# Performance work log

Measured on AMD Instinct MI355X. Metric: run time of the kernel, lower is better.

The kernel has to match this reference:

```python
import jax, jax.numpy as jnp
import numpy as np

N = 800          # atoms
F = 128          # n_filters / embedding dim
G = 50           # n_gaussians
L_INT = 3        # n_interactions
CUTOFF = 5.0     # Angstrom
BOX_NM = 2.3     # box edge in nm (positions are in nm, scaled *10 inside)
LOG2 = 0.6931471805599453


def ssp(x):
    # shifted softplus used throughout schnetpack
    return jax.nn.softplus(x) - LOG2


def setup_inputs() -> dict:
    key = jax.random.key(0)
    ks = jax.random.split(key, 20)
    s = 0.05
    inp = {
        "positions": jax.random.uniform(ks[0], (N, 3), jnp.float32) * BOX_NM,
        "boxvectors": (BOX_NM * jnp.eye(3)).astype(jnp.float32),
        "atomic_numbers": jax.random.randint(ks[1], (N,), 1, 10),
        "embedding": jax.random.normal(ks[2], (100, F), jnp.float32) * s,
        # filter-generating network (per interaction, stacked on leading dim)
        "Wf1": jax.random.normal(ks[3], (L_INT, G, F), jnp.float32) * s,
        "bf1": jnp.zeros((L_INT, F), jnp.float32),
        "Wf2": jax.random.normal(ks[4], (L_INT, F, F), jnp.float32) * s,
        "bf2": jnp.zeros((L_INT, F), jnp.float32),
        # cfconv in2f (no bias) and post-aggregation dense layers
        "Win": jax.random.normal(ks[5], (L_INT, F, F), jnp.float32) * s,
        "W2": jax.random.normal(ks[6], (L_INT, F, F), jnp.float32) * s,
        "b2": jnp.zeros((L_INT, F), jnp.float32),
        "W3": jax.random.normal(ks[7], (L_INT, F, F), jnp.float32) * s,
        "b3": jnp.zeros((L_INT, F), jnp.float32),
        # Atomwise output head (F -> F//2 -> 1)
        "Wo1": jax.random.normal(ks[8], (F, F // 2), jnp.float32) * s,
        "bo1": jnp.zeros((F // 2,), jnp.float32),
        "Wo2": jax.random.normal(ks[9], (F // 2, 1), jnp.float32) * s,
        "bo2": jnp.zeros((1,), jnp.float32),
    }
    return inp


def reference(positions, boxvectors, atomic_numbers, embedding,
              Wf1, bf1, Wf2, bf2, Win, W2, b2, W3, b3,
              Wo1, bo1, Wo2, bo2):
    # nm -> Angstrom, as in the original forward
    pos = positions * 10.0
    cell = boxvectors * 10.0

    # PBC pairwise displacements via minimum image (box > 2*cutoff, so exact
    # equivalent of the shift-based neighbor list within the cutoff)
    d = pos[:, None, :] - pos[None, :, :]                  # [N,N,3]
    inv_cell = jnp.linalg.inv(cell)
    frac = d @ inv_cell
    frac = frac - jnp.round(frac)
    d = frac @ cell

    eye = jnp.eye(pos.shape[0], dtype=bool)
    r2 = jnp.sum(d * d, axis=-1)
    r = jnp.sqrt(jnp.where(eye, 1.0, r2))                  # safe sqrt on diag
    nbr_mask = (r < CUTOFF) & (~eye)                       # neighbor_mask
    fmask = nbr_mask.astype(pos.dtype)

    # gaussian RBF expansion on [0, cutoff]
    centers = jnp.linspace(0.0, CUTOFF, G, dtype=pos.dtype)
    width = centers[1] - centers[0]
    gamma = 0.5 / (width * width)
    g = jnp.exp(-gamma * (r[..., None] - centers) ** 2) * fmask[..., None]  # [N,N,G]

    # SchNet interactions
    x = embedding[atomic_numbers]                           # [N,F]
    for l in range(L_INT):
        # continuous filters W_ij from distances
        Wij = ssp(jnp.einsum('ijg,gf->ijf', g, Wf1[l]) + bf1[l])
        Wij = (jnp.einsum('ijf,fk->ijk', Wij, Wf2[l]) + bf2[l]) * fmask[..., None]
        xf = x @ Win[l]                                     # in2f
        m = jnp.einsum('ijf,jf->if', Wij, xf)               # gather-weight-scatter
        v = ssp(m @ W2[l] + b2[l]) @ W3[l] + b3[l]
        x = x + v                                           # residual update

    # Atomwise energy head, sum-pooled to total potential
    e_atom = ssp(x @ Wo1 + bo1) @ Wo2 + bo2                 # [N,1]
    return jnp.sum(e_atom)
```

## Files before the change

kernel.cpp:

```cpp
#include <hip/hip_runtime.h>

#define SN_NA    800
#define SN_F     128
#define SN_G     50
#define SN_MAXP  16384
#define SN_MAXN  128
#define SN_CUT2  25.0f

typedef __attribute__((ext_vector_type(4))) float f32x4;
typedef __attribute__((ext_vector_type(8))) short short8;

#define OB_BF1 0
#define OB_BF2 384
#define OB_B2  768
#define OB_B3  1152
#define OB_BO1 1536
#define OB_WO2 1600
#define OB_BO2 1664
#define NB_TOT 1665

#define OT_WF1T 0
#define OT_WF2T 24576
#define OT_W2T  73728
#define OT_W3T  122880
#define OT_WINT 172032
#define OT_WO1T 221184
#define NT_TOT  229376

#define WO_PCNT  0
#define WO_DONE  32
#define WO_NCLO  64
#define WO_NCUP  3264
#define WO_NBRP  6464
#define WO_NBRO  416064
#define WO_PAIRR 825664
#define WO_WB    891200
#define WO_WTT   897872
#define WO_WPH   1356624
#define WO_X     13939536
#define WO_XF    14349136
#define WO_XF2   14758736
#define WO_EPART 15168336
#define SN_WSNEED (WO_EPART + 256)

__device__ __forceinline__ float ldr(const void* p, int idx, int bf) {
    if (bf) {
        unsigned int x = ((unsigned int)(((const unsigned short*)p)[idx])) << 16;
        float f; __builtin_memcpy(&f, &x, 4); return f;
    }
    return ((const float*)p)[idx];
}
__device__ __forceinline__ int bfflag(const void* box) {
    float b0 = ((const float*)box)[0];
    return !(b0 > 1e-3f && b0 < 1e3f);
}
__device__ __forceinline__ float bf2f(unsigned short u) {
    unsigned int x = ((unsigned int)u) << 16;
    float f; __builtin_memcpy(&f, &x, 4); return f;
}
__device__ __forceinline__ unsigned short f2bf(float v) {
    unsigned int b; __builtin_memcpy(&b, &v, 4);
    return (unsigned short)((b + 0x7FFFu + ((b >> 16) & 1u)) >> 16);
}
__device__ __forceinline__ float sspf(float v) {
    float sp = fmaxf(v, 0.0f) + log1pf(__expf(-fabsf(v)));
    return sp - 0.69314718055994530942f;
}

__global__ void k_prep(const void* pos, const void* box,
                       const void* bf1w, const void* bf2w, const void* b2m, const void* b3m,
                       const void* bo1w, const void* wo2w, const void* bo2w,
                       const void* wf1, const void* wf2, const void* w2m, const void* w3m,
                       const void* winm, const void* wo1,
                       float* wb, unsigned short* wtT,
                       int* pcnt, int* ncup, int* nclo,
                       int* nbrp, int* nbro, float* pairr) {
    __shared__ int   lj[64];
    __shared__ float lr[64];
    __shared__ int   lsh[2];
    int bf = bfflag(box);
    int bid = blockIdx.x, tid = threadIdx.x;

    if (bid < 7) {
        int t = bid * 256 + tid;
        if (t < NB_TOT) {
            const int   sz[7] = {384,384,384,384,64,64,1};
            const void* ps[7] = {bf1w,bf2w,b2m,b3m,bo1w,wo2w,bo2w};
            int rem = t, s = 0;
#pragma unroll
            for (int q = 0; q < 7; q++) { if (rem >= sz[q]) { rem -= sz[q]; s = q+1; } else break; }
            wb[t] = ldr(ps[s], rem, bf);
        }
        return;
    }
    if (bid < 903) {
        int t = (bid - 7) * 256 + tid;
        if (t < NT_TOT) {
            float v;
            if (t < OT_WF2T) {
                int lay = t / 8192, rem = t - lay*8192, col = rem >> 6, k = rem & 63;
                v = (k < SN_G) ? ldr(wf1, lay*(SN_G*SN_F) + k*SN_F + col, bf) : 0.0f;
            } else if (t < OT_W2T) {
                int i2 = t - OT_WF2T; int lay = i2 >> 14, rem = i2 & 16383, col = rem >> 7, k = rem & 127;
                v = ldr(wf2, lay*16384 + k*128 + col, bf);
            } else if (t < OT_W3T) {
                int i2 = t - OT_W2T;  int lay = i2 >> 14, rem = i2 & 16383, col = rem >> 7, k = rem & 127;
                v = ldr(w2m, lay*16384 + k*128 + col, bf);
            } else if (t < OT_WINT) {
                int i2 = t - OT_W3T;  int lay = i2 >> 14, rem = i2 & 16383, col = rem >> 7, k = rem & 127;
                v = ldr(w3m, lay*16384 + k*128 + col, bf);
            } else if (t < OT_WO1T) {
                int i2 = t - OT_WINT; int lay = i2 >> 14, rem = i2 & 16383, col = rem >> 7, k = rem & 127;
                v = ldr(winm, lay*16384 + k*128 + col, bf);
            } else {
                int i2 = t - OT_WO1T; int col = i2 >> 7, k = i2 & 127;
                v = ldr(wo1, k*64 + col, bf);
            }
            wtT[t] = f2bf(v);
        }
        return;
    }

    int i = bid - 903;
    if (tid == 0) lsh[0] = 0;
    float c00 = ldr(box,0,bf)*10.f, c01 = ldr(box,1,bf)*10.f, c02 = ldr(box,2,bf)*10.f;
    float c10 = ldr(box,3,bf)*10.f, c11 = ldr(box,4,bf)*10.f, c12 = ldr(box,5,bf)*10.f;
    float c20 = ldr(box,6,bf)*10.f, c21 = ldr(box,7,bf)*10.f, c22 = ldr(box,8,bf)*10.f;
    float det = c00*(c11*c22 - c12*c21) - c01*(c10*c22 - c12*c20) + c02*(c10*c21 - c11*c20);
    float id  = 1.0f / det;
    float i00 = (c11*c22 - c12*c21)*id, i01 = (c02*c21 - c01*c22)*id, i02 = (c01*c12 - c02*c11)*id;
    float i10 = (c12*c20 - c10*c22)*id, i11 = (c00*c22 - c02*c20)*id, i12 = (c02*c10 - c00*c12)*id;
    float i20 = (c10*c21 - c11*c20)*id, i21 = (c01*c20 - c00*c21)*id, i22 = (c00*c11 - c01*c10)*id;
    float xi = ldr(pos, i*3+0, bf)*10.f;
    float yi = ldr(pos, i*3+1, bf)*10.f;
    float zi = ldr(pos, i*3+2, bf)*10.f;
    __syncthreads();

    for (int j = i + 1 + tid; j < SN_NA; j += 256) {
        float dx = xi - ldr(pos, j*3+0, bf)*10.f;
        float dy = yi - ldr(pos, j*3+1, bf)*10.f;
        float dz = zi - ldr(pos, j*3+2, bf)*10.f;
        float fx = dx*i00 + dy*i10 + dz*i20;
        float fy = dx*i01 + dy*i11 + dz*i21;
        float fz = dx*i02 + dy*i12 + dz*i22;
        fx -= rintf(fx); fy -= rintf(fy); fz -= rintf(fz);
        float ax = fx*c00 + fy*c10 + fz*c20;
        float ay = fx*c01 + fy*c11 + fz*c21;
        float az = fx*c02 + fy*c12 + fz*c22;
        float r2 = ax*ax + ay*ay + az*az;
        if (r2 < SN_CUT2) {
            int k = atomicAdd(&lsh[0], 1);
            if (k < 64) { lj[k] = j; lr[k] = sqrtf(r2); }
        }
    }
    __syncthreads();

    int cnt = lsh[0]; if (cnt > 64) cnt = 64;
    if (tid == 0) lsh[1] = atomicAdd(pcnt, cnt);
    __syncthreads();
    int base = lsh[1];
    int avail = SN_MAXP - base; if (avail < 0) avail = 0;
    int stored = cnt < avail ? cnt : avail;
    if (tid == 0) ncup[i] = stored;

    if (tid < stored) {
        int p = base + tid;
        int j = lj[tid];
        pairr[p] = lr[tid];
        nbrp[i*SN_MAXN + tid] = p;
        nbro[i*SN_MAXN + tid] = j;
        int kj = atomicAdd(&nclo[j], 1);
        if (kj < 64) {
            nbrp[j*SN_MAXN + 64 + kj] = p;
            nbro[j*SN_MAXN + 64 + kj] = i;
        }
    }
}

__global__ void k_initfilter(const int* zn, const void* emb, const void* box,
                             const float* pairr, const int* pcnt,
                             const float* wb, const unsigned short* wtT,
                             float* x, float* xf, unsigned short* wph) {
    __shared__ unsigned short es[16][136];
    __shared__ unsigned short gls[16][72];
    __shared__ unsigned short hls[16][136];
    int tid  = threadIdx.x;
    int lane = tid & 63;
    int wave = tid >> 6;
    int rowA = lane & 15;
    int kgrp = lane >> 4;

    if (blockIdx.x < 50) {
        int bf = bfflag(box);
        int a0 = blockIdx.x * 16;
        int a = tid >> 4, f0 = (tid & 15) * 8;
        int atom = a0 + a;
        int z = zn[atom];
        float v[8];
#pragma unroll
        for (int q = 0; q < 8; q++) v[q] = ldr(emb, z*SN_F + f0 + q, bf);
        *(float4*)&x[atom*SN_F + f0]     = make_float4(v[0],v[1],v[2],v[3]);
        *(float4*)&x[atom*SN_F + f0 + 4] = make_float4(v[4],v[5],v[6],v[7]);
#pragma unroll
        for (int q = 0; q < 8; q++) es[a][f0+q] = f2bf(v[q]);
        __syncthreads();

        int c0 = wave * 32;
        f32x4 acc0 = {0.f,0.f,0.f,0.f}, acc1 = {0.f,0.f,0.f,0.f};
        const unsigned short* wn = wtT + OT_WINT;
#pragma unroll
        for (int ks = 0; ks < 4; ks++) {
            short8 a8 = *(const short8*)&es[rowA][ks*32 + kgrp*8];
            short8 w0 = *(const short8*)(wn + (c0 + rowA)*128      + ks*32 + kgrp*8);
            short8 w1 = *(const short8*)(wn + (c0 + 16 + rowA)*128 + ks*32 + kgrp*8);
            acc0 = __builtin_amdgcn_mfma_f32_16x16x32_bf16(a8, w0, acc0, 0, 0, 0);
            acc1 = __builtin_amdgcn_mfma_f32_16x16x32_bf16(a8, w1, acc1, 0, 0, 0);
        }
#pragma unroll
        for (int r = 0; r < 4; r++) {
            int row = kgrp*4 + r;
            xf[(a0 + row)*SN_F + c0 + rowA]      = acc0[r];
            xf[(a0 + row)*SN_F + c0 + 16 + rowA] = acc1[r];
        }
        return;
    }

    int fb  = blockIdx.x - 50;
    int lay = fb >> 10;
    int p0  = (fb & 1023) * 16;
    int cnt = *pcnt; if (cnt > SN_MAXP) cnt = SN_MAXP;
    if (p0 >= cnt) return;
    int c0 = wave * 32;

    {
        int pr = tid >> 4, k0 = (tid & 15) * 4;
        int p = p0 + pr;
        float r = (p < cnt) ? pairr[p] : -1.0f;
        const float width = 5.0f/49.0f, gamma = 0.5f/(width*width);
        unsigned short gv[4];
#pragma unroll
        for (int q = 0; q < 4; q++) {
            int k = k0 + q;
            float g = 0.f;
            if (k < SN_G && r >= 0.f) { float d = r - width*(float)k; g = __expf(-gamma*d*d); }
            gv[q] = f2bf(g);
        }
        *(unsigned long long*)&gls[pr][k0] = *(unsigned long long*)gv;
    }
    __syncthreads();

    f32x4 acc0 = {0.f,0.f,0.f,0.f}, acc1 = {0.f,0.f,0.f,0.f};
    const unsigned short* b1 = wtT + OT_WF1T + lay*8192;
#pragma unroll
    for (int ks = 0; ks < 2; ks++) {
        short8 a8 = *(const short8*)&gls[rowA][ks*32 + kgrp*8];
        short8 w0 = *(const short8*)(b1 + (c0 + rowA)*64      + ks*32 + kgrp*8);
        short8 w1 = *(const short8*)(b1 + (c0 + 16 + rowA)*64 + ks*32 + kgrp*8);
        acc0 = __builtin_amdgcn_mfma_f32_16x16x32_bf16(a8, w0, acc0, 0, 0, 0);
        acc1 = __builtin_amdgcn_mfma_f32_16x16x32_bf16(a8, w1, acc1, 0, 0, 0);
    }
    {
        float b1c0 = wb[OB_BF1 + lay*SN_F + c0 + rowA];
        float b1c1 = wb[OB_BF1 + lay*SN_F + c0 + 16 + rowA];
#pragma unroll
        for (int r = 0; r < 4; r++) {
            int row = kgrp*4 + r;
            hls[row][c0 + rowA]      = f2bf(sspf(acc0[r] + b1c0));
            hls[row][c0 + 16 + rowA] = f2bf(sspf(acc1[r] + b1c1));
        }
    }
    __syncthreads();

    f32x4 d0 = {0.f,0.f,0.f,0.f}, d1 = {0.f,0.f,0.f,0.f};
    const unsigned short* b2w = wtT + OT_WF2T + lay*16384;
#pragma unroll
    for (int ks = 0; ks < 4; ks++) {
        short8 a8 = *(const short8*)&hls[rowA][ks*32 + kgrp*8];
        short8 w0 = *(const short8*)(b2w + (c0 + rowA)*128      + ks*32 + kgrp*8);
        short8 w1 = *(const short8*)(b2w + (c0 + 16 + rowA)*128 + ks*32 + kgrp*8);
        d0 = __builtin_amdgcn_mfma_f32_16x16x32_bf16(a8, w0, d0, 0, 0, 0);
        d1 = __builtin_amdgcn_mfma_f32_16x16x32_bf16(a8, w1, d1, 0, 0, 0);
    }
    {
        unsigned short* wout = wph + lay*(SN_MAXP*SN_F);
        float b2c0 = wb[OB_BF2 + lay*SN_F + c0 + rowA];
        float b2c1 = wb[OB_BF2 + lay*SN_F + c0 + 16 + rowA];
#pragma unroll
        for (int r = 0; r < 4; r++) {
            int p = p0 + kgrp*4 + r;
            wout[p*SN_F + c0 + rowA]      = f2bf(d0[r] + b2c0);
            wout[p*SN_F + c0 + 16 + rowA] = f2bf(d1[r] + b2c1);
        }
    }
}

__global__ void k_layerM(const int* ncup, const int* nclo,
                         const int* nbrp, const int* nbro,
                         const unsigned short* wph, const float* xf_in, float* x,
                         const float* wb, const unsigned short* wtT,
                         int lay, int layNext, float* xf_out,
                         float* epart, int* done, const void* box, void* out) {
    __shared__ int   spA[16][128], sjA[16][128];
    __shared__ unsigned short ms[16][136], ts[16][136], xs[16][136];
    __shared__ float red[512];
    __shared__ int   lastf;
    int tid = threadIdx.x;
    int a0 = blockIdx.x * 16;
    int a = tid >> 5, l32 = tid & 31;
    int atom = a0 + a;
    int up = ncup[atom]; if (up > 64) up = 64;
    int lo = nclo[atom]; if (lo > 64) lo = 64;
    int cn = up + lo;
    for (int k = l32; k < up; k += 32) {
        spA[a][k] = nbrp[atom*SN_MAXN + k];
        sjA[a][k] = nbro[atom*SN_MAXN + k];
    }
    for (int k = l32; k < lo; k += 32) {
        spA[a][up + k] = nbrp[atom*SN_MAXN + 64 + k];
        sjA[a][up + k] = nbro[atom*SN_MAXN + 64 + k];
    }
    __syncthreads();

    {
        int f0 = l32 * 4;
        float acc[4] = {0.f,0.f,0.f,0.f};
        const unsigned short* wpb = wph + lay*(SN_MAXP*SN_F);
        int k = 0;
        for (; k + 2 <= cn; k += 2) {
            int p0 = spA[a][k],   j0 = sjA[a][k];
            int p1 = spA[a][k+1], j1 = sjA[a][k+1];
            ushort4 w0 = *(const ushort4*)(wpb + p0*SN_F + f0);
            ushort4 w1 = *(const ushort4*)(wpb + p1*SN_F + f0);
            float4  xa = *(const float4*)(xf_in + j0*SN_F + f0);
            float4  xb = *(const float4*)(xf_in + j1*SN_F + f0);
            acc[0] = fmaf(bf2f(w0.x), xa.x, fmaf(bf2f(w1.x), xb.x, acc[0]));
            acc[1] = fmaf(bf2f(w0.y), xa.y, fmaf(bf2f(w1.y), xb.y, acc[1]));
            acc[2] = fmaf(bf2f(w0.z), xa.z, fmaf(bf2f(w1.z), xb.z, acc[2]));
            acc[3] = fmaf(bf2f(w0.w), xa.w, fmaf(bf2f(w1.w), xb.w, acc[3]));
        }
        if (k < cn) {
            int p0 = spA[a][k], j0 = sjA[a][k];
            ushort4 w0 = *(const ushort4*)(wpb + p0*SN_F + f0);
            float4  xa = *(const float4*)(xf_in + j0*SN_F + f0);
            acc[0] = fmaf(bf2f(w0.x), xa.x, acc[0]);
            acc[1] = fmaf(bf2f(w0.y), xa.y, acc[1]);
            acc[2] = fmaf(bf2f(w0.z), xa.z, acc[2]);
            acc[3] = fmaf(bf2f(w0.w), xa.w, acc[3]);
        }
#pragma unroll
        for (int q = 0; q < 4; q++) ms[a][f0+q] = f2bf(acc[q]);
    }
    __syncthreads();

    int lane = tid & 63;
    int wave = tid >> 6;
    int c0   = wave * 16;
    int rowA = lane & 15;
    int kgrp = lane >> 4;
    int col  = c0 + rowA;

    {
        f32x4 acc = {0.f,0.f,0.f,0.f};
        const unsigned short* w = wtT + OT_W2T + lay*16384;
#pragma unroll
        for (int ks = 0; ks < 4; ks++) {
            short8 a8 = *(const short8*)&ms[rowA][ks*32 + kgrp*8];
            short8 w8 = *(const short8*)(w + col*128 + ks*32 + kgrp*8);
            acc = __builtin_amdgcn_mfma_f32_16x16x32_bf16(a8, w8, acc, 0, 0, 0);
        }
        float bc = wb[OB_B2 + lay*SN_F + col];
#pragma unroll
        for (int r = 0; r < 4; r++) ts[kgrp*4 + r][col] = f2bf(sspf(acc[r] + bc));
    }
    __syncthreads();

    {
        f32x4 acc = {0.f,0.f,0.f,0.f};
        const unsigned short* w = wtT + OT_W3T + lay*16384;
#pragma unroll
        for (int ks = 0; ks < 4; ks++) {
            short8 a8 = *(const short8*)&ts[rowA][ks*32 + kgrp*8];
            short8 w8 = *(const short8*)(w + col*128 + ks*32 + kgrp*8);
            acc = __builtin_amdgcn_mfma_f32_16x16x32_bf16(a8, w8, acc, 0, 0, 0);
        }
        float bc = wb[OB_B3 + lay*SN_F + col];
#pragma unroll
        for (int r = 0; r < 4; r++) {
            int row = kgrp*4 + r;
            float xnew = x[(a0 + row)*SN_F + col] + acc[r] + bc;
            x[(a0 + row)*SN_F + col] = xnew;
            xs[row][col] = f2bf(xnew);
        }
    }
    __syncthreads();

    if (layNext >= 0) {
        f32x4 acc = {0.f,0.f,0.f,0.f};
        const unsigned short* w = wtT + OT_WINT + layNext*16384;
#pragma unroll
        for (int ks = 0; ks < 4; ks++) {
            short8 a8 = *(const short8*)&xs[rowA][ks*32 + kgrp*8];
            short8 w8 = *(const short8*)(w + col*128 + ks*32 + kgrp*8);
            acc = __builtin_amdgcn_mfma_f32_16x16x32_bf16(a8, w8, acc, 0, 0, 0);
        }
#pragma unroll
        for (int r = 0; r < 4; r++)
            xf_out[(a0 + kgrp*4 + r)*SN_F + col] = acc[r];
        return;
    }

    float e = 0.f;
    if (wave < 4) {
        f32x4 H = {0.f,0.f,0.f,0.f};
        const unsigned short* w = wtT + OT_WO1T;
#pragma unroll
        for (int ks = 0; ks < 4; ks++) {
            short8 a8 = *(const short8*)&xs[rowA][ks*32 + kgrp*8];
            short8 w8 = *(const short8*)(w + col*128 + ks*32 + kgrp*8);
            H = __builtin_amdgcn_mfma_f32_16x16x32_bf16(a8, w8, H, 0, 0, 0);
        }
        float bo = wb[OB_BO1 + col];
        float wo = wb[OB_WO2 + col];
#pragma unroll
        for (int r = 0; r < 4; r++) e += sspf(H[r] + bo) * wo;
    }
    red[tid] = e;
    __syncthreads();
    for (int wd = 256; wd > 0; wd >>= 1) {
        if (tid < wd) red[tid] += red[tid + wd];
        __syncthreads();
    }
    if (tid == 0) {
        epart[blockIdx.x] = red[0];
        __threadfence();
        int old = atomicAdd(done, 1);
        lastf = (old == 49);
    }
    __syncthreads();
    if (lastf) {
        __threadfence();
        if (tid < 64) {
            float s = (tid < 50) ? epart[tid] : 0.f;
#pragma unroll
            for (int off = 32; off > 0; off >>= 1) s += __shfl_down(s, off, 64);
            if (tid == 0) {
                float v = s + (float)SN_NA * wb[OB_BO2];
                if (bfflag(box)) ((unsigned short*)out)[0] = f2bf(v);
                else             ((float*)out)[0] = v;
            }
        }
    }
}

__global__ void k_fail(void* out) {
    ((unsigned short*)out)[0] = 0x449A;
}

extern "C" void kernel_launch(void* const* d_in, const int* in_sizes, int n_in,
                              void* d_out, int out_size, void* d_ws, size_t ws_size,
                              hipStream_t stream)
{
    const void* pos = d_in[0];
    const void* box = d_in[1];
    const int*  zn  = (const int*)d_in[2];
    const void* emb = d_in[3];

    if (ws_size < (size_t)SN_WSNEED) {
        k_fail<<<1, 1, 0, stream>>>(d_out);
        return;
    }

    char* ws = (char*)d_ws;
    int*            pcnt  = (int*)           (ws + WO_PCNT);
    int*            done  = (int*)           (ws + WO_DONE);
    int*            nclo  = (int*)           (ws + WO_NCLO);
    int*            ncup  = (int*)           (ws + WO_NCUP);
    int*            nbrp  = (int*)           (ws + WO_NBRP);
    int*            nbro  = (int*)           (ws + WO_NBRO);
    float*          pairr = (float*)         (ws + WO_PAIRR);
    float*          wb    = (float*)         (ws + WO_WB);
    unsigned short* wtT   = (unsigned short*)(ws + WO_WTT);
    unsigned short* wph   = (unsigned short*)(ws + WO_WPH);
    float*          x     = (float*)         (ws + WO_X);
    float*          xfA   = (float*)         (ws + WO_XF);
    float*          xfB   = (float*)         (ws + WO_XF2);
    float*          epart = (float*)         (ws + WO_EPART);

    hipMemsetAsync(ws, 0, 3264, stream);

    k_prep<<<1703, 256, 0, stream>>>(pos, box,
        d_in[5], d_in[7], d_in[10], d_in[12], d_in[14], d_in[15], d_in[16],
        d_in[4], d_in[6], d_in[9], d_in[11], d_in[8], d_in[13],
        wb, wtT, pcnt, ncup, nclo, nbrp, nbro, pairr);

    k_initfilter<<<50 + 3*1024, 256, 0, stream>>>(zn, emb, box, pairr, pcnt,
                                                  wb, wtT, x, xfA, wph);

    float* xf_in = xfA;
    float* xf_out = xfB;
    for (int l = 0; l < 3; l++) {
        int layNext = (l < 2) ? (l + 1) : -1;
        k_layerM<<<50, 512, 0, stream>>>(ncup, nclo, nbrp, nbro, wph, xf_in, x,
                                         wb, wtT, l, layNext, xf_out,
                                         epart, done, box, d_out);
        float* t = xf_in; xf_in = xf_out; xf_out = t;
    }
}
```

Baseline: 95.79 us.

## Pack neighbor lists and split layer kernel into 100 blocks of 8 atoms

The pair index and neighbor atom index are packed into a single 32-bit word, which halves neighbor-list storage and the loads needed to fill it. The per-layer kernel now runs 100 blocks of 256 threads, each covering 8 atoms instead of 16, so twice as many CUs take part in the memory-bound gather phase. The MFMA stages now compute 32 columns per wave and zero-pad the unused 8 rows of the 16-row tile, which wastes half the matrix work. The final energy reduction is adapted to 100 partial sums.

```diff
diff --git a/kernel.cpp b/kernel.cpp
--- a/kernel.cpp
+++ b/kernel.cpp
@@ -31,8 +31,7 @@
 #define WO_DONE  32
 #define WO_NCLO  64
 #define WO_NCUP  3264
-#define WO_NBRP  6464
-#define WO_NBRO  416064
+#define WO_NBR   6464
 #define WO_PAIRR 825664
 #define WO_WB    891200
 #define WO_WTT   897872
@@ -41,7 +40,7 @@
 #define WO_XF    14349136
 #define WO_XF2   14758736
 #define WO_EPART 15168336
-#define SN_WSNEED (WO_EPART + 256)
+#define SN_WSNEED (WO_EPART + 512)
 
 __device__ __forceinline__ float ldr(const void* p, int idx, int bf) {
     if (bf) {
@@ -74,7 +73,7 @@
                        const void* winm, const void* wo1,
                        float* wb, unsigned short* wtT,
                        int* pcnt, int* ncup, int* nclo,
-                       int* nbrp, int* nbro, float* pairr) {
+                       unsigned int* nbr, float* pairr) {
     __shared__ int   lj[64];
     __shared__ float lr[64];
     __shared__ int   lsh[2];
@@ -167,13 +166,9 @@
         int p = base + tid;
         int j = lj[tid];
         pairr[p] = lr[tid];
-        nbrp[i*SN_MAXN + tid] = p;
-        nbro[i*SN_MAXN + tid] = j;
+        nbr[i*SN_MAXN + tid] = ((unsigned int)p << 10) | (unsigned int)j;
         int kj = atomicAdd(&nclo[j], 1);
-        if (kj < 64) {
-            nbrp[j*SN_MAXN + 64 + kj] = p;
-            nbro[j*SN_MAXN + 64 + kj] = i;
-        }
+        if (kj < 64) nbr[j*SN_MAXN + 64 + kj] = ((unsigned int)p << 10) | (unsigned int)i;
     }
 }
 
@@ -295,30 +290,28 @@
 }
 
 __global__ void k_layerM(const int* ncup, const int* nclo,
-                         const int* nbrp, const int* nbro,
+                         const unsigned int* nbr,
                          const unsigned short* wph, const float* xf_in, float* x,
                          const float* wb, const unsigned short* wtT,
                          int lay, int layNext, float* xf_out,
                          float* epart, int* done, const void* box, void* out) {
-    __shared__ int   spA[16][128], sjA[16][128];
+    __shared__ unsigned int nl[8][128];
     __shared__ unsigned short ms[16][136], ts[16][136], xs[16][136];
-    __shared__ float red[512];
+    __shared__ float red[256];
     __shared__ int   lastf;
     int tid = threadIdx.x;
-    int a0 = blockIdx.x * 16;
+    int a0 = blockIdx.x * 8;
     int a = tid >> 5, l32 = tid & 31;
     int atom = a0 + a;
     int up = ncup[atom]; if (up > 64) up = 64;
     int lo = nclo[atom]; if (lo > 64) lo = 64;
     int cn = up + lo;
-    for (int k = l32; k < up; k += 32) {
-        spA[a][k] = nbrp[atom*SN_MAXN + k];
-        sjA[a][k] = nbro[atom*SN_MAXN + k];
-    }
-    for (int k = l32; k < lo; k += 32) {
-        spA[a][up + k] = nbrp[atom*SN_MAXN + 64 + k];
-        sjA[a][up + k] = nbro[atom*SN_MAXN + 64 + k];
-    }
+    for (int k = l32; k < up; k += 32) nl[a][k]      = nbr[atom*SN_MAXN + k];
+    for (int k = l32; k < lo; k += 32) nl[a][up + k] = nbr[atom*SN_MAXN + 64 + k];
+    ms[8 + (tid >> 5)][(tid & 31)*4 + 0] = 0;
+    ms[8 + (tid >> 5)][(tid & 31)*4 + 1] = 0;
+    ms[8 + (tid >> 5)][(tid & 31)*4 + 2] = 0;
+    ms[8 + (tid >> 5)][(tid & 31)*4 + 3] = 0;
     __syncthreads();
 
     {
@@ -327,21 +320,20 @@
         const unsigned short* wpb = wph + lay*(SN_MAXP*SN_F);
         int k = 0;
         for (; k + 2 <= cn; k += 2) {
-            int p0 = spA[a][k],   j0 = sjA[a][k];
-            int p1 = spA[a][k+1], j1 = sjA[a][k+1];
-            ushort4 w0 = *(const ushort4*)(wpb + p0*SN_F + f0);
-            ushort4 w1 = *(const ushort4*)(wpb + p1*SN_F + f0);
-            float4  xa = *(const float4*)(xf_in + j0*SN_F + f0);
-            float4  xb = *(const float4*)(xf_in + j1*SN_F + f0);
+            unsigned int v0 = nl[a][k], v1 = nl[a][k+1];
+            ushort4 w0 = *(const ushort4*)(wpb + (v0 >> 10)*SN_F + f0);
+            ushort4 w1 = *(const ushort4*)(wpb + (v1 >> 10)*SN_F + f0);
+            float4  xa = *(const float4*)(xf_in + (v0 & 1023)*SN_F + f0);
+            float4  xb = *(const float4*)(xf_in + (v1 & 1023)*SN_F + f0);
             acc[0] = fmaf(bf2f(w0.x), xa.x, fmaf(bf2f(w1.x), xb.x, acc[0]));
             acc[1] = fmaf(bf2f(w0.y), xa.y, fmaf(bf2f(w1.y), xb.y, acc[1]));
             acc[2] = fmaf(bf2f(w0.z), xa.z, fmaf(bf2f(w1.z), xb.z, acc[2]));
             acc[3] = fmaf(bf2f(w0.w), xa.w, fmaf(bf2f(w1.w), xb.w, acc[3]));
         }
         if (k < cn) {
-            int p0 = spA[a][k], j0 = sjA[a][k];
-            ushort4 w0 = *(const ushort4*)(wpb + p0*SN_F + f0);
-            float4  xa = *(const float4*)(xf_in + j0*SN_F + f0);
+            unsigned int v0 = nl[a][k];
+            ushort4 w0 = *(const ushort4*)(wpb + (v0 >> 10)*SN_F + f0);
+            float4  xa = *(const float4*)(xf_in + (v0 & 1023)*SN_F + f0);
             acc[0] = fmaf(bf2f(w0.x), xa.x, acc[0]);
             acc[1] = fmaf(bf2f(w0.y), xa.y, acc[1]);
             acc[2] = fmaf(bf2f(w0.z), xa.z, acc[2]);
@@ -354,63 +346,88 @@
 
     int lane = tid & 63;
     int wave = tid >> 6;
-    int c0   = wave * 16;
+    int c0   = wave * 32;
     int rowA = lane & 15;
     int kgrp = lane >> 4;
-    int col  = c0 + rowA;
-
-    {
-        f32x4 acc = {0.f,0.f,0.f,0.f};
+
+    {
+        f32x4 A0 = {0.f,0.f,0.f,0.f}, A1 = {0.f,0.f,0.f,0.f};
         const unsigned short* w = wtT + OT_W2T + lay*16384;
 #pragma unroll
         for (int ks = 0; ks < 4; ks++) {
             short8 a8 = *(const short8*)&ms[rowA][ks*32 + kgrp*8];
-            short8 w8 = *(const short8*)(w + col*128 + ks*32 + kgrp*8);
-            acc = __builtin_amdgcn_mfma_f32_16x16x32_bf16(a8, w8, acc, 0, 0, 0);
-        }
-        float bc = wb[OB_B2 + lay*SN_F + col];
-#pragma unroll
-        for (int r = 0; r < 4; r++) ts[kgrp*4 + r][col] = f2bf(sspf(acc[r] + bc));
-    }
-    __syncthreads();
-
-    {
-        f32x4 acc = {0.f,0.f,0.f,0.f};
+            short8 w0 = *(const short8*)(w + (c0 + rowA)*128      + ks*32 + kgrp*8);
+            short8 w1 = *(const short8*)(w + (c0 + 16 + rowA)*128 + ks*32 + kgrp*8);
+            A0 = __builtin_amdgcn_mfma_f32_16x16x32_bf16(a8, w0, A0, 0, 0, 0);
+            A1 = __builtin_amdgcn_mfma_f32_16x16x32_bf16(a8, w1, A1, 0, 0, 0);
+        }
+        float bc0 = wb[OB_B2 + lay*SN_F + c0 + rowA];
+        float bc1 = wb[OB_B2 + lay*SN_F + c0 + 16 + rowA];
+#pragma unroll
+        for (int r = 0; r < 4; r++) {
+            int row = kgrp*4 + r;
+            ts[row][c0 + rowA]      = f2bf(sspf(A0[r] + bc0));
+            ts[row][c0 + 16 + rowA] = f2bf(sspf(A1[r] + bc1));
+        }
+    }
+    __syncthreads();
+
+    {
+        f32x4 A0 = {0.f,0.f,0.f,0.f}, A1 = {0.f,0.f,0.f,0.f};
         const unsigned short* w = wtT + OT_W3T + lay*16384;
 #pragma unroll
         for (int ks = 0; ks < 4; ks++) {
             short8 a8 = *(const short8*)&ts[rowA][ks*32 + kgrp*8];
-            short8 w8 = *(const short8*)(w + col*128 + ks*32 + kgrp*8);
-            acc = __builtin_amdgcn_mfma_f32_16x16x32_bf16(a8, w8, acc, 0, 0, 0);
-        }
-        float bc = wb[OB_B3 + lay*SN_F + col];
+            short8 w0 = *(const short8*)(w + (c0 + rowA)*128      + ks*32 + kgrp*8);
+            short8 w1 = *(const short8*)(w + (c0 + 16 + rowA)*128 + ks*32 + kgrp*8);
+            A0 = __builtin_amdgcn_mfma_f32_16x16x32_bf16(a8, w0, A0, 0, 0, 0);
+            A1 = __builtin_amdgcn_mfma_f32_16x16x32_bf16(a8, w1, A1, 0, 0, 0);
+        }
+        float bc0 = wb[OB_B3 + lay*SN_F + c0 + rowA];
+        float bc1 = wb[OB_B3 + lay*SN_F + c0 + 16 + rowA];
 #pragma unroll
         for (int r = 0; r < 4; r++) {
             int row = kgrp*4 + r;
-            float xnew = x[(a0 + row)*SN_F + col] + acc[r] + bc;
-            x[(a0 + row)*SN_F + col] = xnew;
-            xs[row][col] = f2bf(xnew);
+            if (row < 8) {
+                float xn0 = x[(a0 + row)*SN_F + c0 + rowA]      + A0[r] + bc0;
+                float xn1 = x[(a0 + row)*SN_F + c0 + 16 + rowA] + A1[r] + bc1;
+                x[(a0 + row)*SN_F + c0 + rowA]      = xn0;
+                x[(a0 + row)*SN_F + c0 + 16 + rowA] = xn1;
+                xs[row][c0 + rowA]      = f2bf(xn0);
+                xs[row][c0 + 16 + rowA] = f2bf(xn1);
+            } else {
+                xs[row][c0 + rowA]      = 0;
+                xs[row][c0 + 16 + rowA] = 0;
+            }
         }
     }
     __syncthreads();
 
     if (layNext >= 0) {
-        f32x4 acc = {0.f,0.f,0.f,0.f};
+        f32x4 A0 = {0.f,0.f,0.f,0.f}, A1 = {0.f,0.f,0.f,0.f};
         const unsigned short* w = wtT + OT_WINT + layNext*16384;
 #pragma unroll
         for (int ks = 0; ks < 4; ks++) {
             short8 a8 = *(const short8*)&xs[rowA][ks*32 + kgrp*8];
-            short8 w8 = *(const short8*)(w + col*128 + ks*32 + kgrp*8);
-            acc = __builtin_amdgcn_mfma_f32_16x16x32_bf16(a8, w8, acc, 0, 0, 0);
-        }
-#pragma unroll
-        for (int r = 0; r < 4; r++)
-            xf_out[(a0 + kgrp*4 + r)*SN_F + col] = acc[r];
+            short8 w0 = *(const short8*)(w + (c0 + rowA)*128      + ks*32 + kgrp*8);
+            short8 w1 = *(const short8*)(w + (c0 + 16 + rowA)*128 + ks*32 + kgrp*8);
+            A0 = __builtin_amdgcn_mfma_f32_16x16x32_bf16(a8, w0, A0, 0, 0, 0);
+            A1 = __builtin_amdgcn_mfma_f32_16x16x32_bf16(a8, w1, A1, 0, 0, 0);
+        }
+#pragma unroll
+        for (int r = 0; r < 4; r++) {
+            int row = kgrp*4 + r;
+            if (row < 8) {
+                xf_out[(a0 + row)*SN_F + c0 + rowA]      = A0[r];
+                xf_out[(a0 + row)*SN_F + c0 + 16 + rowA] = A1[r];
+            }
+        }
         return;
     }
 
     float e = 0.f;
-    if (wave < 4) {
+    {
+        int col = wave*16 + rowA;
         f32x4 H = {0.f,0.f,0.f,0.f};
         const unsigned short* w = wtT + OT_WO1T;
 #pragma unroll
@@ -419,14 +436,16 @@
             short8 w8 = *(const short8*)(w + col*128 + ks*32 + kgrp*8);
             H = __builtin_amdgcn_mfma_f32_16x16x32_bf16(a8, w8, H, 0, 0, 0);
         }
-        float bo = wb[OB_BO1 + col];
-        float wo = wb[OB_WO2 + col];
-#pragma unroll
-        for (int r = 0; r < 4; r++) e += sspf(H[r] + bo) * wo;
+        if (kgrp < 2) {
+            float bo = wb[OB_BO1 + col];
+            float wo = wb[OB_WO2 + col];
+#pragma unroll
+            for (int r = 0; r < 4; r++) e += sspf(H[r] + bo) * wo;
+        }
     }
     red[tid] = e;
     __syncthreads();
-    for (int wd = 256; wd > 0; wd >>= 1) {
+    for (int wd = 128; wd > 0; wd >>= 1) {
         if (tid < wd) red[tid] += red[tid + wd];
         __syncthreads();
     }
@@ -434,20 +453,21 @@
         epart[blockIdx.x] = red[0];
         __threadfence();
         int old = atomicAdd(done, 1);
-        lastf = (old == 49);
+        lastf = (old == 99);
     }
     __syncthreads();
     if (lastf) {
         __threadfence();
-        if (tid < 64) {
-            float s = (tid < 50) ? epart[tid] : 0.f;
-#pragma unroll
-            for (int off = 32; off > 0; off >>= 1) s += __shfl_down(s, off, 64);
-            if (tid == 0) {
-                float v = s + (float)SN_NA * wb[OB_BO2];
-                if (bfflag(box)) ((unsigned short*)out)[0] = f2bf(v);
-                else             ((float*)out)[0] = v;
-            }
+        red[tid] = (tid < 100) ? epart[tid] : 0.f;
+        __syncthreads();
+        for (int wd = 128; wd > 0; wd >>= 1) {
+            if (tid < wd) red[tid] += red[tid + wd];
+            __syncthreads();
+        }
+        if (tid == 0) {
+            float v = red[0] + (float)SN_NA * wb[OB_BO2];
+            if (bfflag(box)) ((unsigned short*)out)[0] = f2bf(v);
+            else             ((float*)out)[0] = v;
         }
     }
 }
@@ -475,8 +495,7 @@
     int*            done  = (int*)           (ws + WO_DONE);
     int*            nclo  = (int*)           (ws + WO_NCLO);
     int*            ncup  = (int*)           (ws + WO_NCUP);
-    int*            nbrp  = (int*)           (ws + WO_NBRP);
-    int*            nbro  = (int*)           (ws + WO_NBRO);
+    unsigned int*   nbr   = (unsigned int*)  (ws + WO_NBR);
     float*          pairr = (float*)         (ws + WO_PAIRR);
     float*          wb    = (float*)         (ws + WO_WB);
     unsigned short* wtT   = (unsigned short*)(ws + WO_WTT);
@@ -491,7 +510,7 @@
     k_prep<<<1703, 256, 0, stream>>>(pos, box,
         d_in[5], d_in[7], d_in[10], d_in[12], d_in[14], d_in[15], d_in[16],
         d_in[4], d_in[6], d_in[9], d_in[11], d_in[8], d_in[13],
-        wb, wtT, pcnt, ncup, nclo, nbrp, nbro, pairr);
+        wb, wtT, pcnt, ncup, nclo, nbr, pairr);
 
     k_initfilter<<<50 + 3*1024, 256, 0, stream>>>(zn, emb, box, pairr, pcnt,
                                                   wb, wtT, x, xfA, wph);
@@ -500,9 +519,9 @@
     float* xf_out = xfB;
     for (int l = 0; l < 3; l++) {
         int layNext = (l < 2) ? (l + 1) : -1;
-        k_layerM<<<50, 512, 0, stream>>>(ncup, nclo, nbrp, nbro, wph, xf_in, x,
-                                         wb, wtT, l, layNext, xf_out,
-                                         epart, done, box, d_out);
+        k_layerM<<<100, 256, 0, stream>>>(ncup, nclo, nbr, wph, xf_in, x,
+                                          wb, wtT, l, layNext, xf_out,
+                                          epart, done, box, d_out);
         float* t = xf_in; xf_in = xf_out; xf_out = t;
     }
 }
```

After: 96.28 us. No clear change (+0.5%).
